# Kernel optimization log

Hardware: AMD Instinct MI355X
Metric: run time of the kernel (lower is better)

Reference implementation:

```python
import jax, jax.numpy as jnp
import numpy as np

HID = 128
N_BATCH = 16384


def gru_cell(x, h, Wih, Whh, bih, bhh):
    # PyTorch GRUCell: weight_ih [3H, in], weight_hh [3H, H], gate order r,z,n
    gi = x @ Wih.T + bih            # [N, 3H]
    gh = h @ Whh.T + bhh            # [N, 3H]
    ir, iz, ic = jnp.split(gi, 3, axis=-1)
    hr, hz, hc = jnp.split(gh, 3, axis=-1)
    r = jax.nn.sigmoid(ir + hr)
    z = jax.nn.sigmoid(iz + hz)
    c = jnp.tanh(ic + r * hc)
    return (1.0 - z) * c + z * h


def setup_inputs() -> dict:
    key = jax.random.key(0)
    ks = jax.random.split(key, 11)
    s = 0.05  # small init like uniform(-1/sqrt(H), 1/sqrt(H))
    return {
        "x": jax.random.normal(ks[0], (N_BATCH, 1, 28, 28), jnp.float32),
        "Wih1": jax.random.normal(ks[1], (3 * HID, 28), jnp.float32) * s,
        "Whh1": jax.random.normal(ks[2], (3 * HID, HID), jnp.float32) * s,
        "bih1": jax.random.normal(ks[3], (3 * HID,), jnp.float32) * s,
        "bhh1": jax.random.normal(ks[4], (3 * HID,), jnp.float32) * s,
        "Wih2": jax.random.normal(ks[5], (3 * HID, HID), jnp.float32) * s,
        "Whh2": jax.random.normal(ks[6], (3 * HID, HID), jnp.float32) * s,
        "bih2": jax.random.normal(ks[7], (3 * HID,), jnp.float32) * s,
        "bhh2": jax.random.normal(ks[8], (3 * HID,), jnp.float32) * s,
        "Wout": jax.random.normal(ks[9], (10, HID), jnp.float32) * s,
        "bout": jax.random.normal(ks[10], (10,), jnp.float32) * s,
    }


def reference(x, Wih1, Whh1, bih1, bhh1, Wih2, Whh2, bih2, bhh2, Wout, bout):
    n, c, h, w = x.shape
    xs = x.transpose(0, 2, 1, 3).reshape(n, h, w * c)  # [N, T=28, 28]
    xs = jnp.swapaxes(xs, 0, 1)                        # [T, N, 28]
    h1_0 = jnp.zeros((n, HID), x.dtype)
    zeros_h = jnp.zeros((n, HID), x.dtype)  # cell2 gets a fresh zero hidden each step (bug in source, kept)

    def step(h1, xt):
        h0 = jax.nn.relu(gru_cell(xt, h1, Wih1, Whh1, bih1, bhh1))
        h1_new = gru_cell(h0, zeros_h, Wih2, Whh2, bih2, bhh2)
        return h1_new, None

    h1, _ = jax.lax.scan(step, h1_0, xs)
    return h1 @ Wout.T + bout  # [N, 10]
```

## Files before the change

### kernel.cpp

```cpp
#include <hip/hip_runtime.h>
#include <hip/hip_bf16.h>
#include <stdint.h>

#define HID 128
#define NB 16384
#define TSTEPS 28
#define BN 64

typedef __attribute__((ext_vector_type(8))) short s16x8;
typedef __attribute__((ext_vector_type(4))) float f32x4;

#define H1_OFF 0
#define H0_OFF 17408
#define XT_OFF 34816
#define WI2_OFF 45056
#define SMEM_BYTES 143360
#define HSTRIDE 272
#define RFSTRIDE 4352
#define XSTRIDE 80

#define L2E 1.442695041f
#define TL2E 2.885390082f

__device__ __forceinline__ unsigned cvtpk2(float lo, float hi) {
  unsigned r;
  asm("v_cvt_pk_bf16_f32 %0, %1, %2" : "=v"(r) : "v"(lo), "v"(hi));
  return r;
}
__device__ __forceinline__ float sig_pre(float acc, float nb) {
  float e = __builtin_amdgcn_exp2f(fmaf(acc, -L2E, nb));
  return __builtin_amdgcn_rcpf(1.0f + e);
}
__device__ __forceinline__ float tanh_nc(float x) {
  float e2 = __builtin_amdgcn_exp2f(x * TL2E);
  float q = __builtin_amdgcn_rcpf(1.0f + e2);
  return fmaf(-2.0f, q, 1.0f);
}

__global__ __launch_bounds__(512, 1) void gru_kernel(
    const float* __restrict__ x,
    const float* __restrict__ Wih1, const float* __restrict__ Whh1,
    const float* __restrict__ bih1, const float* __restrict__ bhh1,
    const float* __restrict__ Wih2,
    const float* __restrict__ bih2, const float* __restrict__ bhh2,
    const float* __restrict__ Wout, const float* __restrict__ bout,
    float* __restrict__ out)
{
  __shared__ char smem[SMEM_BYTES];
  const int tid = threadIdx.x;
  const int wv   = tid >> 6;
  const int lane = tid & 63;
  const int l15 = lane & 15;
  const int l16 = lane >> 4;
  const int hc0 = wv * 16;
  const int n0 = blockIdx.x * BN;

  f32x4 zq = {0.f, 0.f, 0.f, 0.f};
  asm("" : "+v"(zq));

  const int hrd = l15 * HSTRIDE + l16 * 16;
  const int hwr = (4 * l16) * HSTRIDE + (hc0 + l15) * 2;
  const int srow = tid >> 4, skp = tid & 15;
  const int xrd = XT_OFF + l15 * XSTRIDE + l16 * 16;
  const int xwr = XT_OFF + srow * XSTRIDE + skp * 4;
  const int wib = WI2_OFF + wv * 12288 + lane * 16;

  s16x8 fw_hh1[4][3];
  s16x8 fw_ih1[3];
  const int gb0 = hc0, gb1 = 128 + hc0, gb2 = 256 + hc0;
  #pragma unroll
  for (int kf = 0; kf < 4; ++kf) {
    int kbase = kf * 32 + l16 * 8;
    #pragma unroll
    for (int cb = 0; cb < 3; ++cb) {
      int g = (cb == 0 ? gb0 : cb == 1 ? gb1 : gb2) + l15;
      const float* p1 = Whh1 + g * HID + kbase;
      const float* p2 = Wih2 + g * HID + kbase;
      s16x8 f1, f2;
      #pragma unroll
      for (int j = 0; j < 8; j += 2) {
        unsigned u1 = cvtpk2(p1[j], p1[j + 1]);
        unsigned u2 = cvtpk2(p2[j], p2[j + 1]);
        f1[j] = (short)u1; f1[j + 1] = (short)(u1 >> 16);
        f2[j] = (short)u2; f2[j + 1] = (short)(u2 >> 16);
      }
      fw_hh1[kf][cb] = f1;
      *(s16x8*)(smem + wib + (kf * 3 + cb) * 1024) = f2;
    }
  }
  {
    int kbase = l16 * 8;
    #pragma unroll
    for (int cb = 0; cb < 3; ++cb) {
      int g = (cb == 0 ? gb0 : cb == 1 ? gb1 : gb2) + l15;
      s16x8 f;
      #pragma unroll
      for (int j = 0; j < 8; ++j) {
        int k = kbase + j;
        f[j] = (k < 28) ? (short)cvtpk2(Wih1[g * 28 + k], 0.f) : (short)0;
      }
      fw_ih1[cb] = f;
    }
  }
  const float nb_r  = -L2E * (bih1[gb0 + l15] + bhh1[gb0 + l15]);
  const float nb_z  = -L2E * (bih1[gb1 + l15] + bhh1[gb1 + l15]);
  const float b_ci  = bih1[gb2 + l15];
  const float b_ch  = bhh1[gb2 + l15];
  const float nb_r2 = -L2E * (bih2[gb0 + l15] + bhh2[gb0 + l15]);
  const float nb_z2 = -L2E * (bih2[gb1 + l15] + bhh2[gb1 + l15]);
  const float c_c2  = bih2[gb2 + l15];
  const float c_hc2 = bhh2[gb2 + l15];

  float h1reg[4][4];
  #pragma unroll
  for (int rf = 0; rf < 4; ++rf)
    #pragma unroll
    for (int j = 0; j < 4; ++j) h1reg[rf][j] = 0.f;

  const float2* xp0 = (const float2*)(x + (size_t)(n0 + srow) * 784 + 2 * skp);
  const float2* xp1 = (const float2*)(x + (size_t)(n0 + srow + 32) * 784 + 2 * skp);

  {
    float2 v0 = make_float2(0.f, 0.f), v1 = make_float2(0.f, 0.f);
    if (skp < 14) { v0 = *xp0; v1 = *xp1; }
    xp0 += 14; xp1 += 14;
    *(unsigned*)(smem + xwr)        = cvtpk2(v0.x, v0.y);
    *(unsigned*)(smem + xwr + 2560) = cvtpk2(v1.x, v1.y);
  }
  #pragma unroll
  for (int i = 0; i < 3; ++i) {
    int idx = tid + i * 512;
    if (idx < 1088) ((int4*)(smem + H1_OFF))[idx] = make_int4(0, 0, 0, 0);
  }
  __syncthreads();

  #pragma unroll 1
  for (int t = 0; t < TSTEPS; ++t) {
    const int xb = (t & 1) * 5120;
    #pragma unroll
    for (int rf = 0; rf < 4; ++rf) {
      s16x8 ax = *(const s16x8*)(smem + xrd + xb + rf * 1280);
      s16x8 ah[4];
      #pragma unroll
      for (int kf = 0; kf < 4; ++kf)
        ah[kf] = *(const s16x8*)(smem + H1_OFF + hrd + rf * RFSTRIDE + kf * 64);
      f32x4 aR, aZ, aCi, aCh;
      aR  = __builtin_amdgcn_mfma_f32_16x16x32_bf16(ax, fw_ih1[0], zq, 0, 0, 0);
      aZ  = __builtin_amdgcn_mfma_f32_16x16x32_bf16(ax, fw_ih1[1], zq, 0, 0, 0);
      aCi = __builtin_amdgcn_mfma_f32_16x16x32_bf16(ax, fw_ih1[2], zq, 0, 0, 0);
      aCh = __builtin_amdgcn_mfma_f32_16x16x32_bf16(ah[0], fw_hh1[0][2], zq, 0, 0, 0);
      #pragma unroll
      for (int kf = 0; kf < 4; ++kf) {
        aR = __builtin_amdgcn_mfma_f32_16x16x32_bf16(ah[kf], fw_hh1[kf][0], aR, 0, 0, 0);
        aZ = __builtin_amdgcn_mfma_f32_16x16x32_bf16(ah[kf], fw_hh1[kf][1], aZ, 0, 0, 0);
        if (kf > 0)
          aCh = __builtin_amdgcn_mfma_f32_16x16x32_bf16(ah[kf], fw_hh1[kf][2], aCh, 0, 0, 0);
      }
      float h0v[4];
      #pragma unroll
      for (int j = 0; j < 4; ++j) {
        float r = sig_pre(aR[j], nb_r);
        float z = sig_pre(aZ[j], nb_z);
        float c = tanh_nc(fmaf(r, aCh[j] + b_ch, aCi[j] + b_ci));
        h0v[j] = fmaxf(fmaf(z, h1reg[rf][j] - c, c), 0.f);
      }
      unsigned pk01 = cvtpk2(h0v[0], h0v[1]);
      unsigned pk23 = cvtpk2(h0v[2], h0v[3]);
      *(short*)(smem + H0_OFF + hwr + rf * RFSTRIDE + 0 * HSTRIDE) = (short)pk01;
      *(short*)(smem + H0_OFF + hwr + rf * RFSTRIDE + 1 * HSTRIDE) = (short)(pk01 >> 16);
      *(short*)(smem + H0_OFF + hwr + rf * RFSTRIDE + 2 * HSTRIDE) = (short)pk23;
      *(short*)(smem + H0_OFF + hwr + rf * RFSTRIDE + 3 * HSTRIDE) = (short)(pk23 >> 16);
    }
    __syncthreads();

    float2 xv0 = make_float2(0.f, 0.f), xv1 = make_float2(0.f, 0.f);
    const bool do_stage = (t + 1 < TSTEPS);
    if (do_stage && skp < 14) { xv0 = *xp0; xv1 = *xp1; }
    xp0 += 14; xp1 += 14;
    #pragma unroll
    for (int rfh = 0; rfh < 2; ++rfh) {
      f32x4 aR2[2], aZ2[2], aC2[2];
      #pragma unroll
      for (int kf = 0; kf < 4; ++kf) {
        s16x8 a0 = *(const s16x8*)(smem + H0_OFF + hrd + rfh * 8704 + kf * 64);
        s16x8 a1 = *(const s16x8*)(smem + H0_OFF + hrd + rfh * 8704 + RFSTRIDE + kf * 64);
        s16x8 b0 = *(const s16x8*)(smem + wib + (kf * 3 + 0) * 1024);
        s16x8 b1 = *(const s16x8*)(smem + wib + (kf * 3 + 1) * 1024);
        s16x8 b2 = *(const s16x8*)(smem + wib + (kf * 3 + 2) * 1024);
        if (kf == 0) {
          aR2[0] = __builtin_amdgcn_mfma_f32_16x16x32_bf16(a0, b0, zq, 0, 0, 0);
          aR2[1] = __builtin_amdgcn_mfma_f32_16x16x32_bf16(a1, b0, zq, 0, 0, 0);
          aZ2[0] = __builtin_amdgcn_mfma_f32_16x16x32_bf16(a0, b1, zq, 0, 0, 0);
          aZ2[1] = __builtin_amdgcn_mfma_f32_16x16x32_bf16(a1, b1, zq, 0, 0, 0);
          aC2[0] = __builtin_amdgcn_mfma_f32_16x16x32_bf16(a0, b2, zq, 0, 0, 0);
          aC2[1] = __builtin_amdgcn_mfma_f32_16x16x32_bf16(a1, b2, zq, 0, 0, 0);
        } else {
          aR2[0] = __builtin_amdgcn_mfma_f32_16x16x32_bf16(a0, b0, aR2[0], 0, 0, 0);
          aR2[1] = __builtin_amdgcn_mfma_f32_16x16x32_bf16(a1, b0, aR2[1], 0, 0, 0);
          aZ2[0] = __builtin_amdgcn_mfma_f32_16x16x32_bf16(a0, b1, aZ2[0], 0, 0, 0);
          aZ2[1] = __builtin_amdgcn_mfma_f32_16x16x32_bf16(a1, b1, aZ2[1], 0, 0, 0);
          aC2[0] = __builtin_amdgcn_mfma_f32_16x16x32_bf16(a0, b2, aC2[0], 0, 0, 0);
          aC2[1] = __builtin_amdgcn_mfma_f32_16x16x32_bf16(a1, b2, aC2[1], 0, 0, 0);
        }
      }
      #pragma unroll
      for (int p = 0; p < 2; ++p) {
        const int rf = rfh * 2 + p;
        float hv[4];
        #pragma unroll
        for (int j = 0; j < 4; ++j) {
          float r2 = sig_pre(aR2[p][j], nb_r2);
          float z2 = sig_pre(aZ2[p][j], nb_z2);
          float c2 = tanh_nc(fmaf(r2, c_hc2, aC2[p][j] + c_c2));
          float h1n = fmaf(-z2, c2, c2);
          h1reg[rf][j] = h1n;
          hv[j] = h1n;
        }
        unsigned pk01 = cvtpk2(hv[0], hv[1]);
        unsigned pk23 = cvtpk2(hv[2], hv[3]);
        *(short*)(smem + H1_OFF + hwr + rf * RFSTRIDE + 0 * HSTRIDE) = (short)pk01;
        *(short*)(smem + H1_OFF + hwr + rf * RFSTRIDE + 1 * HSTRIDE) = (short)(pk01 >> 16);
        *(short*)(smem + H1_OFF + hwr + rf * RFSTRIDE + 2 * HSTRIDE) = (short)pk23;
        *(short*)(smem + H1_OFF + hwr + rf * RFSTRIDE + 3 * HSTRIDE) = (short)(pk23 >> 16);
      }
    }
    if (do_stage) {
      const int xo = 5120 - xb;
      *(unsigned*)(smem + xwr + xo)        = cvtpk2(xv0.x, xv0.y);
      *(unsigned*)(smem + xwr + xo + 2560) = cvtpk2(xv1.x, xv1.y);
    }
    __syncthreads();
  }

  float* houtf = (float*)smem;
  #pragma unroll
  for (int rf = 0; rf < 4; ++rf)
    #pragma unroll
    for (int j = 0; j < 4; ++j) {
      int row = rf * 16 + l16 * 4 + j;
      houtf[row * 132 + hc0 + l15] = h1reg[rf][j];
    }
  __syncthreads();
  for (int task = tid; task < BN * 10; task += 512) {
    int row = task & 63;
    int o = task >> 6;
    const float* hp = houtf + row * 132;
    const float* wp = Wout + o * HID;
    float s = bout[o];
    #pragma unroll 8
    for (int j2 = 0; j2 < HID; ++j2) s = fmaf(hp[j2], wp[j2], s);
    out[(size_t)(n0 + row) * 10 + o] = s;
  }
}

extern "C" void kernel_launch(void* const* d_in, const int* in_sizes, int n_in,
                              void* d_out, int out_size, void* d_ws, size_t ws_size,
                              hipStream_t stream) {
  const float* x    = (const float*)d_in[0];
  const float* Wih1 = (const float*)d_in[1];
  const float* Whh1 = (const float*)d_in[2];
  const float* bih1 = (const float*)d_in[3];
  const float* bhh1 = (const float*)d_in[4];
  const float* Wih2 = (const float*)d_in[5];
  const float* bih2 = (const float*)d_in[7];
  const float* bhh2 = (const float*)d_in[8];
  const float* Wout = (const float*)d_in[9];
  const float* bout = (const float*)d_in[10];
  gru_kernel<<<NB / BN, 512, 0, stream>>>(x, Wih1, Whh1, bih1, bhh1,
                                          Wih2, bih2, bhh2, Wout, bout,
                                          (float*)d_out);
}
```

Measured before the change: 154.4 us.

## Split batch rows across two wave groups with 1024-thread blocks

```diff
diff --git a/kernel.cpp b/kernel.cpp
--- a/kernel.cpp
+++ b/kernel.cpp
@@ -37,7 +37,7 @@
   return fmaf(-2.0f, q, 1.0f);
 }
 
-__global__ __launch_bounds__(512, 1) void gru_kernel(
+__global__ __launch_bounds__(1024, 1) void gru_kernel(
     const float* __restrict__ x,
     const float* __restrict__ Wih1, const float* __restrict__ Whh1,
     const float* __restrict__ bih1, const float* __restrict__ bhh1,
@@ -48,22 +48,24 @@
 {
   __shared__ char smem[SMEM_BYTES];
   const int tid = threadIdx.x;
-  const int wv   = tid >> 6;
+  const int wv16 = tid >> 6;
+  const int mh   = wv16 >> 3;
+  const int cw   = wv16 & 7;
   const int lane = tid & 63;
   const int l15 = lane & 15;
   const int l16 = lane >> 4;
-  const int hc0 = wv * 16;
+  const int hc0 = cw * 16;
   const int n0 = blockIdx.x * BN;
 
   f32x4 zq = {0.f, 0.f, 0.f, 0.f};
   asm("" : "+v"(zq));
 
-  const int hrd = l15 * HSTRIDE + l16 * 16;
-  const int hwr = (4 * l16) * HSTRIDE + (hc0 + l15) * 2;
+  const int hrd = (mh * 32 + l15) * HSTRIDE + l16 * 16;
+  const int hwr = (mh * 32 + 4 * l16) * HSTRIDE + (hc0 + l15) * 2;
   const int srow = tid >> 4, skp = tid & 15;
-  const int xrd = XT_OFF + l15 * XSTRIDE + l16 * 16;
+  const int xrd = XT_OFF + (mh * 32 + l15) * XSTRIDE + l16 * 16;
   const int xwr = XT_OFF + srow * XSTRIDE + skp * 4;
-  const int wib = WI2_OFF + wv * 12288 + lane * 16;
+  const int wib = WI2_OFF + cw * 12288 + lane * 16;
 
   s16x8 fw_hh1[4][3];
   s16x8 fw_ih1[3];
@@ -75,17 +77,23 @@
     for (int cb = 0; cb < 3; ++cb) {
       int g = (cb == 0 ? gb0 : cb == 1 ? gb1 : gb2) + l15;
       const float* p1 = Whh1 + g * HID + kbase;
-      const float* p2 = Wih2 + g * HID + kbase;
-      s16x8 f1, f2;
+      s16x8 f1;
       #pragma unroll
       for (int j = 0; j < 8; j += 2) {
         unsigned u1 = cvtpk2(p1[j], p1[j + 1]);
-        unsigned u2 = cvtpk2(p2[j], p2[j + 1]);
         f1[j] = (short)u1; f1[j + 1] = (short)(u1 >> 16);
-        f2[j] = (short)u2; f2[j + 1] = (short)(u2 >> 16);
       }
       fw_hh1[kf][cb] = f1;
-      *(s16x8*)(smem + wib + (kf * 3 + cb) * 1024) = f2;
+      if (mh == 0) {
+        const float* p2 = Wih2 + g * HID + kbase;
+        s16x8 f2;
+        #pragma unroll
+        for (int j = 0; j < 8; j += 2) {
+          unsigned u2 = cvtpk2(p2[j], p2[j + 1]);
+          f2[j] = (short)u2; f2[j + 1] = (short)(u2 >> 16);
+        }
+        *(s16x8*)(smem + wib + (kf * 3 + cb) * 1024) = f2;
+      }
     }
   }
   {
@@ -111,50 +119,42 @@
   const float c_c2  = bih2[gb2 + l15];
   const float c_hc2 = bhh2[gb2 + l15];
 
-  float h1reg[4][4];
+  float h1reg[2][4];
   #pragma unroll
-  for (int rf = 0; rf < 4; ++rf)
+  for (int rf = 0; rf < 2; ++rf)
     #pragma unroll
     for (int j = 0; j < 4; ++j) h1reg[rf][j] = 0.f;
 
   const float2* xp0 = (const float2*)(x + (size_t)(n0 + srow) * 784 + 2 * skp);
-  const float2* xp1 = (const float2*)(x + (size_t)(n0 + srow + 32) * 784 + 2 * skp);
 
   {
-    float2 v0 = make_float2(0.f, 0.f), v1 = make_float2(0.f, 0.f);
-    if (skp < 14) { v0 = *xp0; v1 = *xp1; }
-    xp0 += 14; xp1 += 14;
-    *(unsigned*)(smem + xwr)        = cvtpk2(v0.x, v0.y);
-    *(unsigned*)(smem + xwr + 2560) = cvtpk2(v1.x, v1.y);
-  }
-  #pragma unroll
-  for (int i = 0; i < 3; ++i) {
-    int idx = tid + i * 512;
-    if (idx < 1088) ((int4*)(smem + H1_OFF))[idx] = make_int4(0, 0, 0, 0);
-  }
+    float2 v0 = make_float2(0.f, 0.f);
+    if (skp < 14) v0 = *xp0;
+    xp0 += 14;
+    *(unsigned*)(smem + xwr) = cvtpk2(v0.x, v0.y);
+  }
+  ((int4*)(smem + H1_OFF))[tid] = make_int4(0, 0, 0, 0);
+  if (tid < 64) ((int4*)(smem + H1_OFF))[tid + 1024] = make_int4(0, 0, 0, 0);
   __syncthreads();
 
   #pragma unroll 1
   for (int t = 0; t < TSTEPS; ++t) {
     const int xb = (t & 1) * 5120;
     #pragma unroll
-    for (int rf = 0; rf < 4; ++rf) {
+    for (int rf = 0; rf < 2; ++rf) {
       s16x8 ax = *(const s16x8*)(smem + xrd + xb + rf * 1280);
-      s16x8 ah[4];
-      #pragma unroll
-      for (int kf = 0; kf < 4; ++kf)
-        ah[kf] = *(const s16x8*)(smem + H1_OFF + hrd + rf * RFSTRIDE + kf * 64);
       f32x4 aR, aZ, aCi, aCh;
       aR  = __builtin_amdgcn_mfma_f32_16x16x32_bf16(ax, fw_ih1[0], zq, 0, 0, 0);
       aZ  = __builtin_amdgcn_mfma_f32_16x16x32_bf16(ax, fw_ih1[1], zq, 0, 0, 0);
       aCi = __builtin_amdgcn_mfma_f32_16x16x32_bf16(ax, fw_ih1[2], zq, 0, 0, 0);
-      aCh = __builtin_amdgcn_mfma_f32_16x16x32_bf16(ah[0], fw_hh1[0][2], zq, 0, 0, 0);
       #pragma unroll
       for (int kf = 0; kf < 4; ++kf) {
-        aR = __builtin_amdgcn_mfma_f32_16x16x32_bf16(ah[kf], fw_hh1[kf][0], aR, 0, 0, 0);
-        aZ = __builtin_amdgcn_mfma_f32_16x16x32_bf16(ah[kf], fw_hh1[kf][1], aZ, 0, 0, 0);
-        if (kf > 0)
-          aCh = __builtin_amdgcn_mfma_f32_16x16x32_bf16(ah[kf], fw_hh1[kf][2], aCh, 0, 0, 0);
+        s16x8 ah = *(const s16x8*)(smem + H1_OFF + hrd + rf * RFSTRIDE + kf * 64);
+        aR = __builtin_amdgcn_mfma_f32_16x16x32_bf16(ah, fw_hh1[kf][0], aR, 0, 0, 0);
+        aZ = __builtin_amdgcn_mfma_f32_16x16x32_bf16(ah, fw_hh1[kf][1], aZ, 0, 0, 0);
+        aCh = (kf == 0)
+            ? __builtin_amdgcn_mfma_f32_16x16x32_bf16(ah, fw_hh1[0][2], zq, 0, 0, 0)
+            : __builtin_amdgcn_mfma_f32_16x16x32_bf16(ah, fw_hh1[kf][2], aCh, 0, 0, 0);
       }
       float h0v[4];
       #pragma unroll
@@ -173,77 +173,65 @@
     }
     __syncthreads();
 
-    float2 xv0 = make_float2(0.f, 0.f), xv1 = make_float2(0.f, 0.f);
+    float2 xv0 = make_float2(0.f, 0.f);
     const bool do_stage = (t + 1 < TSTEPS);
-    if (do_stage && skp < 14) { xv0 = *xp0; xv1 = *xp1; }
-    xp0 += 14; xp1 += 14;
-    #pragma unroll
-    for (int rfh = 0; rfh < 2; ++rfh) {
-      f32x4 aR2[2], aZ2[2], aC2[2];
+    if (do_stage && skp < 14) xv0 = *xp0;
+    xp0 += 14;
+    #pragma unroll
+    for (int p = 0; p < 2; ++p) {
+      f32x4 aR2, aZ2, aC2;
       #pragma unroll
       for (int kf = 0; kf < 4; ++kf) {
-        s16x8 a0 = *(const s16x8*)(smem + H0_OFF + hrd + rfh * 8704 + kf * 64);
-        s16x8 a1 = *(const s16x8*)(smem + H0_OFF + hrd + rfh * 8704 + RFSTRIDE + kf * 64);
+        s16x8 a0 = *(const s16x8*)(smem + H0_OFF + hrd + p * RFSTRIDE + kf * 64);
         s16x8 b0 = *(const s16x8*)(smem + wib + (kf * 3 + 0) * 1024);
         s16x8 b1 = *(const s16x8*)(smem + wib + (kf * 3 + 1) * 1024);
         s16x8 b2 = *(const s16x8*)(smem + wib + (kf * 3 + 2) * 1024);
         if (kf == 0) {
-          aR2[0] = __builtin_amdgcn_mfma_f32_16x16x32_bf16(a0, b0, zq, 0, 0, 0);
-          aR2[1] = __builtin_amdgcn_mfma_f32_16x16x32_bf16(a1, b0, zq, 0, 0, 0);
-          aZ2[0] = __builtin_amdgcn_mfma_f32_16x16x32_bf16(a0, b1, zq, 0, 0, 0);
-          aZ2[1] = __builtin_amdgcn_mfma_f32_16x16x32_bf16(a1, b1, zq, 0, 0, 0);
-          aC2[0] = __builtin_amdgcn_mfma_f32_16x16x32_bf16(a0, b2, zq, 0, 0, 0);
-          aC2[1] = __builtin_amdgcn_mfma_f32_16x16x32_bf16(a1, b2, zq, 0, 0, 0);
+          aR2 = __builtin_amdgcn_mfma_f32_16x16x32_bf16(a0, b0, zq, 0, 0, 0);
+          aZ2 = __builtin_amdgcn_mfma_f32_16x16x32_bf16(a0, b1, zq, 0, 0, 0);
+          aC2 = __builtin_amdgcn_mfma_f32_16x16x32_bf16(a0, b2, zq, 0, 0, 0);
         } else {
-          aR2[0] = __builtin_amdgcn_mfma_f32_16x16x32_bf16(a0, b0, aR2[0], 0, 0, 0);
-          aR2[1] = __builtin_amdgcn_mfma_f32_16x16x32_bf16(a1, b0, aR2[1], 0, 0, 0);
-          aZ2[0] = __builtin_amdgcn_mfma_f32_16x16x32_bf16(a0, b1, aZ2[0], 0, 0, 0);
-          aZ2[1] = __builtin_amdgcn_mfma_f32_16x16x32_bf16(a1, b1, aZ2[1], 0, 0, 0);
-          aC2[0] = __builtin_amdgcn_mfma_f32_16x16x32_bf16(a0, b2, aC2[0], 0, 0, 0);
-          aC2[1] = __builtin_amdgcn_mfma_f32_16x16x32_bf16(a1, b2, aC2[1], 0, 0, 0);
+          aR2 = __builtin_amdgcn_mfma_f32_16x16x32_bf16(a0, b0, aR2, 0, 0, 0);
+          aZ2 = __builtin_amdgcn_mfma_f32_16x16x32_bf16(a0, b1, aZ2, 0, 0, 0);
+          aC2 = __builtin_amdgcn_mfma_f32_16x16x32_bf16(a0, b2, aC2, 0, 0, 0);
         }
       }
-      #pragma unroll
-      for (int p = 0; p < 2; ++p) {
-        const int rf = rfh * 2 + p;
-        float hv[4];
-        #pragma unroll
-        for (int j = 0; j < 4; ++j) {
-          float r2 = sig_pre(aR2[p][j], nb_r2);
-          float z2 = sig_pre(aZ2[p][j], nb_z2);
-          float c2 = tanh_nc(fmaf(r2, c_hc2, aC2[p][j] + c_c2));
-          float h1n = fmaf(-z2, c2, c2);
-          h1reg[rf][j] = h1n;
-          hv[j] = h1n;
-        }
-        unsigned pk01 = cvtpk2(hv[0], hv[1]);
-        unsigned pk23 = cvtpk2(hv[2], hv[3]);
-        *(short*)(smem + H1_OFF + hwr + rf * RFSTRIDE + 0 * HSTRIDE) = (short)pk01;
-        *(short*)(smem + H1_OFF + hwr + rf * RFSTRIDE + 1 * HSTRIDE) = (short)(pk01 >> 16);
-        *(short*)(smem + H1_OFF + hwr + rf * RFSTRIDE + 2 * HSTRIDE) = (short)pk23;
-        *(short*)(smem + H1_OFF + hwr + rf * RFSTRIDE + 3 * HSTRIDE) = (short)(pk23 >> 16);
-      }
+      float hv[4];
+      #pragma unroll
+      for (int j = 0; j < 4; ++j) {
+        float r2 = sig_pre(aR2[j], nb_r2);
+        float z2 = sig_pre(aZ2[j], nb_z2);
+        float c2 = tanh_nc(fmaf(r2, c_hc2, aC2[j] + c_c2));
+        float h1n = fmaf(-z2, c2, c2);
+        h1reg[p][j] = h1n;
+        hv[j] = h1n;
+      }
+      unsigned pk01 = cvtpk2(hv[0], hv[1]);
+      unsigned pk23 = cvtpk2(hv[2], hv[3]);
+      *(short*)(smem + H1_OFF + hwr + p * RFSTRIDE + 0 * HSTRIDE) = (short)pk01;
+      *(short*)(smem + H1_OFF + hwr + p * RFSTRIDE + 1 * HSTRIDE) = (short)(pk01 >> 16);
+      *(short*)(smem + H1_OFF + hwr + p * RFSTRIDE + 2 * HSTRIDE) = (short)pk23;
+      *(short*)(smem + H1_OFF + hwr + p * RFSTRIDE + 3 * HSTRIDE) = (short)(pk23 >> 16);
     }
     if (do_stage) {
       const int xo = 5120 - xb;
-      *(unsigned*)(smem + xwr + xo)        = cvtpk2(xv0.x, xv0.y);
-      *(unsigned*)(smem + xwr + xo + 2560) = cvtpk2(xv1.x, xv1.y);
+      *(unsigned*)(smem + xwr + xo) = cvtpk2(xv0.x, xv0.y);
     }
     __syncthreads();
   }
 
   float* houtf = (float*)smem;
   #pragma unroll
-  for (int rf = 0; rf < 4; ++rf)
+  for (int rf = 0; rf < 2; ++rf)
     #pragma unroll
     for (int j = 0; j < 4; ++j) {
-      int row = rf * 16 + l16 * 4 + j;
+      int row = mh * 32 + rf * 16 + l16 * 4 + j;
       houtf[row * 132 + hc0 + l15] = h1reg[rf][j];
     }
   __syncthreads();
-  for (int task = tid; task < BN * 10; task += 512) {
-    int row = task & 63;
-    int o = task >> 6;
+  if (tid < BN * 10) {
+    int row = tid & 63;
+    int o = tid >> 6;
     const float* hp = houtf + row * 132;
     const float* wp = Wout + o * HID;
     float s = bout[o];
@@ -266,7 +254,7 @@
   const float* bhh2 = (const float*)d_in[8];
   const float* Wout = (const float*)d_in[9];
   const float* bout = (const float*)d_in[10];
-  gru_kernel<<<NB / BN, 512, 0, stream>>>(x, Wih1, Whh1, bih1, bhh1,
-                                          Wih2, bih2, bhh2, Wout, bout,
-                                          (float*)d_out);
-}
+  gru_kernel<<<NB / BN, 1024, 0, stream>>>(x, Wih1, Whh1, bih1, bhh1,
+                                           Wih2, bih2, bhh2, Wout, bout,
+                                           (float*)d_out);
+}
```

Measured after the change: 148.0 us. -4.2%, faster.
